# Kernel optimization log

Hardware: AMD Instinct MI355X
Metric: run time of the kernel (lower is better)

The kernel has to match this reference:

```python
import jax, jax.numpy as jnp
import numpy as np

M = 12288
B = 1
C_IN = 8
C_OUT = 16
K = 5


def setup_inputs() -> dict:
    key = jax.random.key(0)
    kL, kx, kt = jax.random.split(key, 3)
    # Scale L so its spectral radius is ~0.5, keeping L^k x numerically tame.
    L = jax.random.normal(kL, (M, M), dtype=jnp.float32) * (0.5 / np.sqrt(M))
    x = jax.random.normal(kx, (B, C_IN, M), dtype=jnp.float32)
    theta = jax.random.normal(kt, (C_OUT, C_IN, K), dtype=jnp.float32)
    bias = jnp.zeros((1, C_OUT, 1), dtype=jnp.float32)
    return {"L": L, "x": x, "theta": theta, "bias": bias}


def reference(L, x, theta, bias):
    Bb, C_in, Mm = x.shape
    Kk = theta.shape[-1]
    # Batch the shared recurrence L^k x into one (M,M)x(M,B*C_in) matmul per step.
    cur = x.reshape(Bb * C_in, Mm).T          # [M, B*C_in]
    powers = [cur]
    for _ in range(Kk - 1):                   # small fixed K, structural loop
        cur = L @ cur                         # [M, B*C_in]
        powers.append(cur)
    X = jnp.stack(powers, axis=0)             # [K, M, B*C_in]
    X = X.transpose(2, 1, 0).reshape(Bb, C_in, Mm, Kk)  # [B, C_in, M, K]
    y = jnp.einsum('bimk,oik->bom', X, theta)           # [B, C_out, M]
    return y + bias
```

## Files before the change

kernel.cpp:

```cpp
#include <hip/hip_runtime.h>
#include <hip/hip_bf16.h>

#define MM 12288
#define NCH 8
#define COUT 16
#define KK 5
#define ROWS 4

__global__ __launch_bounds__(64) void matpanel_kernel(
        const float* __restrict__ L,
        const float* __restrict__ vin,
        float* __restrict__ vout) {
    const int lane = threadIdx.x;
    const int row0 = blockIdx.x * ROWS;

    float acc[ROWS][NCH];
#pragma unroll
    for (int r = 0; r < ROWS; ++r)
#pragma unroll
        for (int c = 0; c < NCH; ++c) acc[r][c] = 0.f;

    for (int it = 0; it < MM / 256; ++it) {
        const int j = it * 256 + lane * 4;
        float4 v[NCH];
#pragma unroll
        for (int c = 0; c < NCH; ++c)
            v[c] = *(const float4*)(vin + (size_t)c * MM + j);
#pragma unroll
        for (int r = 0; r < ROWS; ++r) {
            const float4 a = *(const float4*)(L + (size_t)(row0 + r) * MM + j);
#pragma unroll
            for (int c = 0; c < NCH; ++c) {
                acc[r][c] += a.x * v[c].x + a.y * v[c].y
                           + a.z * v[c].z + a.w * v[c].w;
            }
        }
    }

    float val[ROWS * NCH];
#pragma unroll
    for (int r = 0; r < ROWS; ++r)
#pragma unroll
        for (int c = 0; c < NCH; ++c) val[r * NCH + c] = acc[r][c];

#pragma unroll
    for (int v = 0; v < 32; ++v) val[v] += __shfl_xor(val[v], 32, 64);

#pragma unroll
    for (int d = 16; d >= 1; d >>= 1) {
        const bool up = (lane & d) != 0;
#pragma unroll
        for (int v = 0; v < 16; ++v) {
            if (v < d) {
                const float keep = up ? val[v + d] : val[v];
                const float send = up ? val[v] : val[v + d];
                const float recv = __shfl_xor(send, d, 64);
                val[v] = keep + recv;
            }
        }
    }

    if (lane < 32) {
        const int r = lane >> 3;
        const int c = lane & 7;
        vout[(size_t)c * MM + row0 + r] = val[0];
    }
}

__global__ __launch_bounds__(256) void combine_kernel(
        const float* __restrict__ x,
        const float* __restrict__ P,
        const float* __restrict__ theta,
        const float* __restrict__ bias,
        float* __restrict__ y) {
    const int m = blockIdx.x * blockDim.x + threadIdx.x;
    if (m >= MM) return;

    float p[KK][NCH];
#pragma unroll
    for (int c = 0; c < NCH; ++c) p[0][c] = x[(size_t)c * MM + m];
#pragma unroll
    for (int k = 1; k < KK; ++k)
#pragma unroll
        for (int c = 0; c < NCH; ++c)
            p[k][c] = P[((size_t)(k - 1) * NCH + c) * MM + m];

#pragma unroll
    for (int o = 0; o < COUT; ++o) {
        float acc = bias[o];
#pragma unroll
        for (int c = 0; c < NCH; ++c)
#pragma unroll
            for (int k = 0; k < KK; ++k)
                acc += theta[(o * NCH + c) * KK + k] * p[k][c];
        y[(size_t)o * MM + m] = acc;
    }
}

extern "C" void kernel_launch(void* const* d_in, const int* in_sizes, int n_in,
                              void* d_out, int out_size, void* d_ws, size_t ws_size,
                              hipStream_t stream) {
    const float* L     = (const float*)d_in[0];
    const float* x     = (const float*)d_in[1];
    const float* theta = (const float*)d_in[2];
    const float* bias  = (const float*)d_in[3];
    float* out = (float*)d_out;
    float* P   = (float*)d_ws;

    const size_t S = (size_t)NCH * MM;
    const int grid = MM / ROWS;

    matpanel_kernel<<<grid, 64, 0, stream>>>(L, x,         P);
    matpanel_kernel<<<grid, 64, 0, stream>>>(L, P,         P + S);
    matpanel_kernel<<<grid, 64, 0, stream>>>(L, P + S,     P + 2 * S);
    matpanel_kernel<<<grid, 64, 0, stream>>>(L, P + 2 * S, P + 3 * S);

    combine_kernel<<<(MM + 255) / 256, 256, 0, stream>>>(x, P, theta, bias, out);
}
```

Baseline: 1.309 ms.

## Stage input vectors in double-buffered LDS shared across 12 waves per block

The matvec kernel now runs 12 waves per block (48 rows), and each wave handles 4 rows as before. The 8-channel input vector is staged cooperatively into a double-buffered shared-memory chunk, with the next chunk prefetched into registers during compute. This cuts the redundant per-wave global reads of the vector, which are L2 traffic competing with the L stream. In exchange it adds two barriers per chunk and 96KB of LDS per block, which limits occupancy.

```diff
diff --git a/kernel.cpp b/kernel.cpp
--- a/kernel.cpp
+++ b/kernel.cpp
@@ -5,14 +5,27 @@
 #define NCH 8
 #define COUT 16
 #define KK 5
+
 #define ROWS 4
+#define WAVES 12
+#define BLOCK (WAVES * 64)
+#define RPB (ROWS * WAVES)
+#define CHUNK 1536
+#define NCHUNK (MM / CHUNK)
+#define F4PC (NCH * CHUNK / 4)
+#define F4PT (F4PC / BLOCK)
+#define C4 (CHUNK / 4)
 
-__global__ __launch_bounds__(64) void matpanel_kernel(
+__global__ __launch_bounds__(BLOCK, 3) void matpanel_kernel(
         const float* __restrict__ L,
         const float* __restrict__ vin,
         float* __restrict__ vout) {
-    const int lane = threadIdx.x;
-    const int row0 = blockIdx.x * ROWS;
+    __shared__ float sv[2][NCH][CHUNK];
+
+    const int tid  = threadIdx.x;
+    const int lane = tid & 63;
+    const int wave = tid >> 6;
+    const int row0 = blockIdx.x * RPB + wave * ROWS;
 
     float acc[ROWS][NCH];
 #pragma unroll
@@ -20,20 +33,70 @@
 #pragma unroll
         for (int c = 0; c < NCH; ++c) acc[r][c] = 0.f;
 
-    for (int it = 0; it < MM / 256; ++it) {
-        const int j = it * 256 + lane * 4;
-        float4 v[NCH];
+    {
+        float4 st[F4PT];
 #pragma unroll
-        for (int c = 0; c < NCH; ++c)
-            v[c] = *(const float4*)(vin + (size_t)c * MM + j);
+        for (int p = 0; p < F4PT; ++p) {
+            const int f  = p * BLOCK + tid;
+            const int ch = f / C4;
+            const int c4 = f % C4;
+            st[p] = *(const float4*)(vin + (size_t)ch * MM + c4 * 4);
+        }
 #pragma unroll
-        for (int r = 0; r < ROWS; ++r) {
-            const float4 a = *(const float4*)(L + (size_t)(row0 + r) * MM + j);
+        for (int p = 0; p < F4PT; ++p) {
+            const int f  = p * BLOCK + tid;
+            const int ch = f / C4;
+            const int c4 = f % C4;
+            *(float4*)(&sv[0][ch][c4 * 4]) = st[p];
+        }
+    }
+    __syncthreads();
+
+    for (int ck = 0; ck < NCHUNK; ++ck) {
+        const int buf   = ck & 1;
+        const int jbase = ck * CHUNK;
+
+        float4 nx[F4PT];
+        if (ck + 1 < NCHUNK) {
 #pragma unroll
-            for (int c = 0; c < NCH; ++c) {
-                acc[r][c] += a.x * v[c].x + a.y * v[c].y
-                           + a.z * v[c].z + a.w * v[c].w;
+            for (int p = 0; p < F4PT; ++p) {
+                const int f  = p * BLOCK + tid;
+                const int ch = f / C4;
+                const int c4 = f % C4;
+                nx[p] = *(const float4*)(vin + (size_t)ch * MM +
+                                         (ck + 1) * CHUNK + c4 * 4);
             }
+        }
+
+#pragma unroll
+        for (int s = 0; s < CHUNK / 256; ++s) {
+            const int jl = s * 256 + lane * 4;
+            float4 v[NCH];
+#pragma unroll
+            for (int c = 0; c < NCH; ++c)
+                v[c] = *(const float4*)(&sv[buf][c][jl]);
+#pragma unroll
+            for (int r = 0; r < ROWS; ++r) {
+                const float4 a =
+                    *(const float4*)(L + (size_t)(row0 + r) * MM + jbase + jl);
+#pragma unroll
+                for (int c = 0; c < NCH; ++c) {
+                    acc[r][c] += a.x * v[c].x + a.y * v[c].y
+                               + a.z * v[c].z + a.w * v[c].w;
+                }
+            }
+        }
+
+        if (ck + 1 < NCHUNK) {
+            __syncthreads();
+#pragma unroll
+            for (int p = 0; p < F4PT; ++p) {
+                const int f  = p * BLOCK + tid;
+                const int ch = f / C4;
+                const int c4 = f % C4;
+                *(float4*)(&sv[buf ^ 1][ch][c4 * 4]) = nx[p];
+            }
+            __syncthreads();
         }
     }
 
@@ -108,12 +171,12 @@
     float* P   = (float*)d_ws;
 
     const size_t S = (size_t)NCH * MM;
-    const int grid = MM / ROWS;
+    const int grid = MM / RPB;
 
-    matpanel_kernel<<<grid, 64, 0, stream>>>(L, x,         P);
-    matpanel_kernel<<<grid, 64, 0, stream>>>(L, P,         P + S);
-    matpanel_kernel<<<grid, 64, 0, stream>>>(L, P + S,     P + 2 * S);
-    matpanel_kernel<<<grid, 64, 0, stream>>>(L, P + 2 * S, P + 3 * S);
+    matpanel_kernel<<<grid, BLOCK, 0, stream>>>(L, x,         P);
+    matpanel_kernel<<<grid, BLOCK, 0, stream>>>(L, P,         P + S);
+    matpanel_kernel<<<grid, BLOCK, 0, stream>>>(L, P + S,     P + 2 * S);
+    matpanel_kernel<<<grid, BLOCK, 0, stream>>>(L, P + 2 * S, P + 3 * S);
 
     combine_kernel<<<(MM + 255) / 256, 256, 0, stream>>>(x, P, theta, bias, out);
 }
```

Measured after the change: 5.120 ms. +291.2%, slower.
